# Kernel optimization log

Hardware: AMD Instinct MI355X
Metric: run time of the kernel (lower is better)

Reference implementation:

```python
import jax, jax.numpy as jnp
import numpy as np

C = 1.0        # curvature
MARGIN = 0.2
NEG_WEIGHT = 0.5
EPS = 1e-15


def poincare_dist(x, y):
    # faithful to Poincare.poincare_dist (including the odd clamp on the ratio)
    x2 = jnp.minimum((x * x).sum(-1), (1.0 - 1e-06) / C)
    y2 = jnp.minimum((y * y).sum(-1), (1.0 - 1e-06) / C)
    diff2 = ((x - y) ** 2).sum(-1)
    num = 2 * C * diff2
    den = (1 - C * x2) * (1 - C * y2)
    z = 1 + jnp.maximum(num / jnp.maximum(den, EPS), 1 + 1e-07)
    return jnp.arccosh(z)


def setup_inputs() -> dict:
    key = jax.random.key(0)
    k1, k2, k3, k4 = jax.random.split(key, 4)
    B, N, L, dh, A = 64, 16, 1024, 64, 8
    # scale so points lie well inside the unit Poincare ball
    h_curr = jax.random.normal(k1, (B, dh), dtype=jnp.float32) * 0.05
    demo_h = jax.random.normal(k2, (B, N, L, dh), dtype=jnp.float32) * 0.05
    n_idx = jax.random.randint(k3, (B, A), 0, N)
    l_idx = jax.random.randint(k4, (B, A), 0, L)  # some lt = l+lookahead will be invalid
    align_idx = jnp.stack([n_idx, l_idx], axis=-1).astype(jnp.int64)
    return {"h_curr": h_curr, "demo_h": demo_h, "align_idx": align_idx, "lookahead": 2}


def reference(h_curr, demo_h, align_idx, lookahead):
    B, dh = h_curr.shape
    _, N, L, _ = demo_h.shape
    A = align_idx.shape[1]

    n0 = align_idx[..., 0].reshape(-1)                     # [B*A]
    l0 = align_idx[..., 1].reshape(-1)
    lt = l0 + lookahead
    valid = (lt >= 0) & (lt < L)                           # [B*A]
    bb = jnp.repeat(jnp.arange(B), A)                      # [B*A]
    lt_c = jnp.clip(lt, 0, L - 1)

    h_now = h_curr[bb]                                     # [B*A, dh]
    h_tgt = demo_h[bb, n0, lt_c]                           # [B*A, dh]
    d_pos = poincare_dist(h_now, h_tgt)                    # [B*A]

    vf = valid.astype(h_curr.dtype)
    n_valid = vf.sum()
    pos_term = (d_pos * vf).sum() / jnp.maximum(n_valid, 1.0)

    # negatives: all steps strictly after lt on the same (b, n) sequence
    seq = demo_h[bb, n0]                                   # [B*A, L, dh]
    d_negs = poincare_dist(h_now[:, None, :], seq)         # [B*A, L]
    neg_mask = (jnp.arange(L)[None, :] > lt[:, None]) & valid[:, None]
    nm = neg_mask.astype(h_curr.dtype)
    hinge = jax.nn.relu(MARGIN - d_negs + d_pos[:, None]) * nm
    cnt = nm.sum(-1)                                       # [B*A]
    per_sample = hinge.sum(-1) / jnp.maximum(cnt, 1.0)
    has_neg = (cnt > 0).astype(h_curr.dtype)
    n_neg_samples = has_neg.sum()
    neg_term = (per_sample * has_neg).sum() / jnp.maximum(n_neg_samples, 1.0)

    return pos_term + NEG_WEIGHT * neg_term
```

## Files before the change

kernel.cpp:

```cpp
#include <hip/hip_runtime.h>
#include <math.h>

#define MARGIN 0.2f
#define NEG_WEIGHT 0.5f

constexpr int Bc = 64, Nc = 16, Lc = 1024, DH = 64, Ac = 8;
constexpr int NSAMP = Bc * Ac;
constexpr int CHUNKS = 16;
constexpr int ROWS_PER_CHUNK = Lc / CHUNKS;
constexpr int WPB = 4;
constexpr int GRID = NSAMP * CHUNKS / WPB;

__device__ __forceinline__ float fast_acosh(float z) {
    return __logf(z + __builtin_sqrtf(z * z - 1.0f));
}

__device__ __forceinline__ float pdist(float x2, float y2, float d2) {
    x2 = fminf(x2, 0.999999f);
    y2 = fminf(y2, 0.999999f);
    float num = 2.0f * d2;
    float den = (1.0f - x2) * (1.0f - y2);
    float ratio = num * __builtin_amdgcn_rcpf(fmaxf(den, 1e-15f));
    float z = 1.0f + fmaxf(ratio, 1.0f + 1e-7f);
    return fast_acosh(z);
}

__global__ __launch_bounds__(256) void sample_kernel(
    const float* __restrict__ h_curr,
    const float* __restrict__ demo_h,
    const int*   __restrict__ align_idx,
    const int*   __restrict__ lookahead_p,
    float* __restrict__ ws)
{
    const int tid  = threadIdx.x;
    const int task = blockIdx.x * WPB + (tid >> 6);
    const int s    = task >> 4;
    const int c    = task & 15;
    const int b    = s >> 3;
    const int lane = tid & 63;
    const int quad = lane & 3;
    const int rg   = lane >> 2;

    const int n0 = align_idx[s * 2 + 0];
    const int l0 = align_idx[s * 2 + 1];
    const int lk = lookahead_p[0];
    const int lt = l0 + lk;
    const bool valid = (lt >= 0) && (lt < Lc);

    if (!valid) {
        if (lane == 0) {
            float* wneg = ws + (size_t)(s * CHUNKS + c) * 2;
            wneg[0] = 0.0f; wneg[1] = 0.0f;
            if (c == 0) {
                float* wpos = ws + (size_t)NSAMP * CHUNKS * 2 + (size_t)s * 2;
                wpos[0] = 0.0f; wpos[1] = 0.0f;
            }
        }
        return;
    }

    const bool dead = (c * ROWS_PER_CHUNK + (ROWS_PER_CHUNK - 1)) <= lt;
    if (dead && c != 0) {
        if (lane == 0) {
            float* wneg = ws + (size_t)(s * CHUNKS + c) * 2;
            wneg[0] = 0.0f; wneg[1] = 0.0f;
        }
        return;
    }

    const int lt_c = min(max(lt, 0), Lc - 1);

    const float* __restrict__ xrow = h_curr + (size_t)b * DH + quad * 16;
    const float* __restrict__ seq  = demo_h + (((size_t)b * Nc + (size_t)n0) * Lc) * DH;

    float4 xv[4];
    #pragma unroll
    for (int j = 0; j < 4; ++j)
        xv[j] = *reinterpret_cast<const float4*>(xrow + j * 4);

    float x2 = 0.0f;
    #pragma unroll
    for (int j = 0; j < 4; ++j) {
        x2 = fmaf(xv[j].x, xv[j].x, x2);
        x2 = fmaf(xv[j].y, xv[j].y, x2);
        x2 = fmaf(xv[j].z, xv[j].z, x2);
        x2 = fmaf(xv[j].w, xv[j].w, x2);
    }
    x2 += __shfl_xor(x2, 1, 64);
    x2 += __shfl_xor(x2, 2, 64);

    float d_pos;
    {
        const float* rowp = seq + (size_t)lt_c * DH + quad * 16;
        float d2 = 0.0f, y2 = 0.0f;
        #pragma unroll
        for (int j = 0; j < 4; ++j) {
            float4 yv = *reinterpret_cast<const float4*>(rowp + j * 4);
            float dx = xv[j].x - yv.x, dy = xv[j].y - yv.y;
            float dz = xv[j].z - yv.z, dw = xv[j].w - yv.w;
            d2 = fmaf(dx, dx, d2); d2 = fmaf(dy, dy, d2);
            d2 = fmaf(dz, dz, d2); d2 = fmaf(dw, dw, d2);
            y2 = fmaf(yv.x, yv.x, y2); y2 = fmaf(yv.y, yv.y, y2);
            y2 = fmaf(yv.z, yv.z, y2); y2 = fmaf(yv.w, yv.w, y2);
        }
        d2 += __shfl_xor(d2, 1, 64); d2 += __shfl_xor(d2, 2, 64);
        y2 += __shfl_xor(y2, 1, 64); y2 += __shfl_xor(y2, 2, 64);
        d_pos = pdist(x2, y2, d2);
    }

    if (dead) {
        if (lane == 0) {
            float* wneg = ws + (size_t)(s * CHUNKS + c) * 2;
            wneg[0] = 0.0f; wneg[1] = 0.0f;
            float* wpos = ws + (size_t)NSAMP * CHUNKS * 2 + (size_t)s * 2;
            wpos[0] = d_pos; wpos[1] = 1.0f;
        }
        return;
    }

    float hinge_acc = 0.0f, cnt_acc = 0.0f;
    #pragma unroll
    for (int it = 0; it < 4; ++it) {
        const int row = c * ROWS_PER_CHUNK + it * 16 + rg;
        const float* rowp = seq + (size_t)row * DH + quad * 16;
        float d2 = 0.0f, y2 = 0.0f;
        #pragma unroll
        for (int j = 0; j < 4; ++j) {
            float4 yv = *reinterpret_cast<const float4*>(rowp + j * 4);
            float dx = xv[j].x - yv.x, dy = xv[j].y - yv.y;
            float dz = xv[j].z - yv.z, dw = xv[j].w - yv.w;
            d2 = fmaf(dx, dx, d2); d2 = fmaf(dy, dy, d2);
            d2 = fmaf(dz, dz, d2); d2 = fmaf(dw, dw, d2);
            y2 = fmaf(yv.x, yv.x, y2); y2 = fmaf(yv.y, yv.y, y2);
            y2 = fmaf(yv.z, yv.z, y2); y2 = fmaf(yv.w, yv.w, y2);
        }
        d2 += __shfl_xor(d2, 1, 64); d2 += __shfl_xor(d2, 2, 64);
        y2 += __shfl_xor(y2, 1, 64); y2 += __shfl_xor(y2, 2, 64);
        float dneg = pdist(x2, y2, d2);
        if (row > lt) {
            hinge_acc += fmaxf(MARGIN - dneg + d_pos, 0.0f);
            cnt_acc   += 1.0f;
        }
    }

    #pragma unroll
    for (int m = 4; m < 64; m <<= 1) {
        hinge_acc += __shfl_xor(hinge_acc, m, 64);
        cnt_acc   += __shfl_xor(cnt_acc,   m, 64);
    }

    if (lane == 0) {
        float* wneg = ws + (size_t)(s * CHUNKS + c) * 2;
        wneg[0] = hinge_acc;
        wneg[1] = cnt_acc;
        if (c == 0) {
            float* wpos = ws + (size_t)NSAMP * CHUNKS * 2 + (size_t)s * 2;
            wpos[0] = d_pos; wpos[1] = 1.0f;
        }
    }
}

__global__ __launch_bounds__(256) void reduce_kernel(
    const float* __restrict__ ws, float* __restrict__ out)
{
    const int tid = threadIdx.x;
    float pn = 0.0f, pv = 0.0f, nn = 0.0f, nc = 0.0f;
    for (int s = tid; s < NSAMP; s += 256) {
        float h = 0.0f, ct = 0.0f;
        #pragma unroll
        for (int c = 0; c < CHUNKS; ++c) {
            h  += ws[(size_t)(s * CHUNKS + c) * 2 + 0];
            ct += ws[(size_t)(s * CHUNKS + c) * 2 + 1];
        }
        float per_sample = h / fmaxf(ct, 1.0f);
        float has_neg = (ct > 0.0f) ? 1.0f : 0.0f;
        nn += per_sample * has_neg;
        nc += has_neg;
        pn += ws[(size_t)NSAMP * CHUNKS * 2 + (size_t)s * 2 + 0];
        pv += ws[(size_t)NSAMP * CHUNKS * 2 + (size_t)s * 2 + 1];
    }
    __shared__ float4 sh[256];
    sh[tid] = make_float4(pn, pv, nn, nc);
    __syncthreads();
    for (int off = 128; off > 0; off >>= 1) {
        if (tid < off) {
            sh[tid].x += sh[tid + off].x;
            sh[tid].y += sh[tid + off].y;
            sh[tid].z += sh[tid + off].z;
            sh[tid].w += sh[tid + off].w;
        }
        __syncthreads();
    }
    if (tid == 0) {
        float pos_term = sh[0].x / fmaxf(sh[0].y, 1.0f);
        float neg_term = sh[0].z / fmaxf(sh[0].w, 1.0f);
        out[0] = pos_term + NEG_WEIGHT * neg_term;
    }
}

extern "C" void kernel_launch(void* const* d_in, const int* in_sizes, int n_in,
                              void* d_out, int out_size, void* d_ws, size_t ws_size,
                              hipStream_t stream) {
    const float* h_curr    = (const float*)d_in[0];
    const float* demo_h    = (const float*)d_in[1];
    const int*   align_idx = (const int*)d_in[2];
    const int*   lookahead = (const int*)d_in[3];
    float* out = (float*)d_out;
    float* ws  = (float*)d_ws;

    sample_kernel<<<GRID, 256, 0, stream>>>(h_curr, demo_h, align_idx, lookahead, ws);
    reduce_kernel<<<1, 256, 0, stream>>>(ws, out);
}
```

Baseline: 24.51 us.

## Assign one full row per lane for negative distances, compute count analytically

The negative-distance loop now gives each lane one whole 64-float row instead of splitting rows across 4-lane quads over 4 iterations. This removes the per-row quad shuffles and turns the count accumulation into a closed-form computation. The cost is that each lane's loads are strided by 256 bytes, which hurts coalescing, and x is reloaded from global memory or cache in full by every lane. Accumulation is split across two chains to expose ILP.

```diff
diff --git a/kernel.cpp b/kernel.cpp
--- a/kernel.cpp
+++ b/kernel.cpp
@@ -7,7 +7,7 @@
 constexpr int Bc = 64, Nc = 16, Lc = 1024, DH = 64, Ac = 8;
 constexpr int NSAMP = Bc * Ac;
 constexpr int CHUNKS = 16;
-constexpr int ROWS_PER_CHUNK = Lc / CHUNKS;
+constexpr int RPC = Lc / CHUNKS;
 constexpr int WPB = 4;
 constexpr int GRID = NSAMP * CHUNKS / WPB;
 
@@ -39,7 +39,6 @@
     const int b    = s >> 3;
     const int lane = tid & 63;
     const int quad = lane & 3;
-    const int rg   = lane >> 2;
 
     const int n0 = align_idx[s * 2 + 0];
     const int l0 = align_idx[s * 2 + 1];
@@ -59,7 +58,7 @@
         return;
     }
 
-    const bool dead = (c * ROWS_PER_CHUNK + (ROWS_PER_CHUNK - 1)) <= lt;
+    const bool dead = (c * RPC + (RPC - 1)) <= lt;
     if (dead && c != 0) {
         if (lane == 0) {
             float* wneg = ws + (size_t)(s * CHUNKS + c) * 2;
@@ -70,13 +69,14 @@
 
     const int lt_c = min(max(lt, 0), Lc - 1);
 
-    const float* __restrict__ xrow = h_curr + (size_t)b * DH + quad * 16;
-    const float* __restrict__ seq  = demo_h + (((size_t)b * Nc + (size_t)n0) * Lc) * DH;
+    const float* __restrict__ xrow_q = h_curr + (size_t)b * DH + quad * 16;
+    const float* __restrict__ xrow   = h_curr + (size_t)b * DH;
+    const float* __restrict__ seq    = demo_h + (((size_t)b * Nc + (size_t)n0) * Lc) * DH;
 
     float4 xv[4];
     #pragma unroll
     for (int j = 0; j < 4; ++j)
-        xv[j] = *reinterpret_cast<const float4*>(xrow + j * 4);
+        xv[j] = *reinterpret_cast<const float4*>(xrow_q + j * 4);
 
     float x2 = 0.0f;
     #pragma unroll
@@ -118,41 +118,55 @@
         return;
     }
 
-    float hinge_acc = 0.0f, cnt_acc = 0.0f;
+    const int row = c * RPC + lane;
+    const float* __restrict__ rowp = seq + (size_t)row * DH;
+    const float ma = MARGIN + d_pos;
+
+    float d2a = 0.0f, d2b = 0.0f, y2a = 0.0f, y2b = 0.0f;
+    #pragma unroll 2
+    for (int dd = 0; dd < 4; ++dd) {
+        float4 xb0 = *reinterpret_cast<const float4*>(xrow + dd * 16 + 0);
+        float4 xb1 = *reinterpret_cast<const float4*>(xrow + dd * 16 + 4);
+        float4 xb2 = *reinterpret_cast<const float4*>(xrow + dd * 16 + 8);
+        float4 xb3 = *reinterpret_cast<const float4*>(xrow + dd * 16 + 12);
+        float4 yb0 = *reinterpret_cast<const float4*>(rowp + dd * 16 + 0);
+        float4 yb1 = *reinterpret_cast<const float4*>(rowp + dd * 16 + 4);
+        float4 yb2 = *reinterpret_cast<const float4*>(rowp + dd * 16 + 8);
+        float4 yb3 = *reinterpret_cast<const float4*>(rowp + dd * 16 + 12);
+
+        float dx;
+        dx = xb0.x - yb0.x; d2a = fmaf(dx, dx, d2a); y2a = fmaf(yb0.x, yb0.x, y2a);
+        dx = xb0.y - yb0.y; d2b = fmaf(dx, dx, d2b); y2b = fmaf(yb0.y, yb0.y, y2b);
+        dx = xb0.z - yb0.z; d2a = fmaf(dx, dx, d2a); y2a = fmaf(yb0.z, yb0.z, y2a);
+        dx = xb0.w - yb0.w; d2b = fmaf(dx, dx, d2b); y2b = fmaf(yb0.w, yb0.w, y2b);
+        dx = xb1.x - yb1.x; d2a = fmaf(dx, dx, d2a); y2a = fmaf(yb1.x, yb1.x, y2a);
+        dx = xb1.y - yb1.y; d2b = fmaf(dx, dx, d2b); y2b = fmaf(yb1.y, yb1.y, y2b);
+        dx = xb1.z - yb1.z; d2a = fmaf(dx, dx, d2a); y2a = fmaf(yb1.z, yb1.z, y2a);
+        dx = xb1.w - yb1.w; d2b = fmaf(dx, dx, d2b); y2b = fmaf(yb1.w, yb1.w, y2b);
+        dx = xb2.x - yb2.x; d2a = fmaf(dx, dx, d2a); y2a = fmaf(yb2.x, yb2.x, y2a);
+        dx = xb2.y - yb2.y; d2b = fmaf(dx, dx, d2b); y2b = fmaf(yb2.y, yb2.y, y2b);
+        dx = xb2.z - yb2.z; d2a = fmaf(dx, dx, d2a); y2a = fmaf(yb2.z, yb2.z, y2a);
+        dx = xb2.w - yb2.w; d2b = fmaf(dx, dx, d2b); y2b = fmaf(yb2.w, yb2.w, y2b);
+        dx = xb3.x - yb3.x; d2a = fmaf(dx, dx, d2a); y2a = fmaf(yb3.x, yb3.x, y2a);
+        dx = xb3.y - yb3.y; d2b = fmaf(dx, dx, d2b); y2b = fmaf(yb3.y, yb3.y, y2b);
+        dx = xb3.z - yb3.z; d2a = fmaf(dx, dx, d2a); y2a = fmaf(yb3.z, yb3.z, y2a);
+        dx = xb3.w - yb3.w; d2b = fmaf(dx, dx, d2b); y2b = fmaf(yb3.w, yb3.w, y2b);
+    }
+    const float d2 = d2a + d2b;
+    const float y2 = y2a + y2b;
+
+    const float dneg = pdist(x2, y2, d2);
+    float h = ((row > lt) ? fmaxf(ma - dneg, 0.0f) : 0.0f);
+
     #pragma unroll
-    for (int it = 0; it < 4; ++it) {
-        const int row = c * ROWS_PER_CHUNK + it * 16 + rg;
-        const float* rowp = seq + (size_t)row * DH + quad * 16;
-        float d2 = 0.0f, y2 = 0.0f;
-        #pragma unroll
-        for (int j = 0; j < 4; ++j) {
-            float4 yv = *reinterpret_cast<const float4*>(rowp + j * 4);
-            float dx = xv[j].x - yv.x, dy = xv[j].y - yv.y;
-            float dz = xv[j].z - yv.z, dw = xv[j].w - yv.w;
-            d2 = fmaf(dx, dx, d2); d2 = fmaf(dy, dy, d2);
-            d2 = fmaf(dz, dz, d2); d2 = fmaf(dw, dw, d2);
-            y2 = fmaf(yv.x, yv.x, y2); y2 = fmaf(yv.y, yv.y, y2);
-            y2 = fmaf(yv.z, yv.z, y2); y2 = fmaf(yv.w, yv.w, y2);
-        }
-        d2 += __shfl_xor(d2, 1, 64); d2 += __shfl_xor(d2, 2, 64);
-        y2 += __shfl_xor(y2, 1, 64); y2 += __shfl_xor(y2, 2, 64);
-        float dneg = pdist(x2, y2, d2);
-        if (row > lt) {
-            hinge_acc += fmaxf(MARGIN - dneg + d_pos, 0.0f);
-            cnt_acc   += 1.0f;
-        }
-    }
-
-    #pragma unroll
-    for (int m = 4; m < 64; m <<= 1) {
-        hinge_acc += __shfl_xor(hinge_acc, m, 64);
-        cnt_acc   += __shfl_xor(cnt_acc,   m, 64);
-    }
+    for (int m = 1; m < 64; m <<= 1)
+        h += __shfl_xor(h, m, 64);
 
     if (lane == 0) {
+        const int cnt = (c + 1) * RPC - max(c * RPC, lt + 1);
         float* wneg = ws + (size_t)(s * CHUNKS + c) * 2;
-        wneg[0] = hinge_acc;
-        wneg[1] = cnt_acc;
+        wneg[0] = h;
+        wneg[1] = (float)cnt;
         if (c == 0) {
             float* wpos = ws + (size_t)NSAMP * CHUNKS * 2 + (size_t)s * 2;
             wpos[0] = d_pos; wpos[1] = 1.0f;
```

New measurement: 33.65 us. +37.3%, slower.

## Remap lanes to 16 per row and skip dead row groups in chunk

Applied to the files above, without the earlier changes.

Each row of 64 floats is now handled by 16 lanes with one float4 each instead of 4 lanes with 16 floats, so a wavefront covers 4 rows per iteration over 16 iterations. Row groups lying entirely at or before the target step are skipped. The negative count is computed in closed form instead of being reduced across lanes. This cuts registers per thread and wasted distance evaluations in partially dead chunks, at the cost of two extra shuffle stages per reduction and a longer, branchy loop.

```diff
diff --git a/kernel.cpp b/kernel.cpp
--- a/kernel.cpp
+++ b/kernel.cpp
@@ -7,7 +7,7 @@
 constexpr int Bc = 64, Nc = 16, Lc = 1024, DH = 64, Ac = 8;
 constexpr int NSAMP = Bc * Ac;
 constexpr int CHUNKS = 16;
-constexpr int ROWS_PER_CHUNK = Lc / CHUNKS;
+constexpr int RPC = Lc / CHUNKS;
 constexpr int WPB = 4;
 constexpr int GRID = NSAMP * CHUNKS / WPB;
 
@@ -38,8 +38,8 @@
     const int c    = task & 15;
     const int b    = s >> 3;
     const int lane = tid & 63;
-    const int quad = lane & 3;
-    const int rg   = lane >> 2;
+    const int gl   = lane & 15;
+    const int rg   = lane >> 4;
 
     const int n0 = align_idx[s * 2 + 0];
     const int l0 = align_idx[s * 2 + 1];
@@ -59,7 +59,7 @@
         return;
     }
 
-    const bool dead = (c * ROWS_PER_CHUNK + (ROWS_PER_CHUNK - 1)) <= lt;
+    const bool dead = (c * RPC + (RPC - 1)) <= lt;
     if (dead && c != 0) {
         if (lane == 0) {
             float* wneg = ws + (size_t)(s * CHUNKS + c) * 2;
@@ -70,41 +70,26 @@
 
     const int lt_c = min(max(lt, 0), Lc - 1);
 
-    const float* __restrict__ xrow = h_curr + (size_t)b * DH + quad * 16;
+    const float* __restrict__ xrow = h_curr + (size_t)b * DH;
     const float* __restrict__ seq  = demo_h + (((size_t)b * Nc + (size_t)n0) * Lc) * DH;
 
-    float4 xv[4];
-    #pragma unroll
-    for (int j = 0; j < 4; ++j)
-        xv[j] = *reinterpret_cast<const float4*>(xrow + j * 4);
-
-    float x2 = 0.0f;
-    #pragma unroll
-    for (int j = 0; j < 4; ++j) {
-        x2 = fmaf(xv[j].x, xv[j].x, x2);
-        x2 = fmaf(xv[j].y, xv[j].y, x2);
-        x2 = fmaf(xv[j].z, xv[j].z, x2);
-        x2 = fmaf(xv[j].w, xv[j].w, x2);
-    }
+    const float4 xq = *reinterpret_cast<const float4*>(xrow + gl * 4);
+    float x2 = fmaf(xq.x, xq.x, fmaf(xq.y, xq.y, fmaf(xq.z, xq.z, xq.w * xq.w)));
     x2 += __shfl_xor(x2, 1, 64);
     x2 += __shfl_xor(x2, 2, 64);
+    x2 += __shfl_xor(x2, 4, 64);
+    x2 += __shfl_xor(x2, 8, 64);
 
     float d_pos;
     {
-        const float* rowp = seq + (size_t)lt_c * DH + quad * 16;
-        float d2 = 0.0f, y2 = 0.0f;
-        #pragma unroll
-        for (int j = 0; j < 4; ++j) {
-            float4 yv = *reinterpret_cast<const float4*>(rowp + j * 4);
-            float dx = xv[j].x - yv.x, dy = xv[j].y - yv.y;
-            float dz = xv[j].z - yv.z, dw = xv[j].w - yv.w;
-            d2 = fmaf(dx, dx, d2); d2 = fmaf(dy, dy, d2);
-            d2 = fmaf(dz, dz, d2); d2 = fmaf(dw, dw, d2);
-            y2 = fmaf(yv.x, yv.x, y2); y2 = fmaf(yv.y, yv.y, y2);
-            y2 = fmaf(yv.z, yv.z, y2); y2 = fmaf(yv.w, yv.w, y2);
-        }
+        const float4 tv = *reinterpret_cast<const float4*>(seq + (size_t)lt_c * DH + gl * 4);
+        float dx = xq.x - tv.x, dy = xq.y - tv.y, dz = xq.z - tv.z, dw = xq.w - tv.w;
+        float d2 = fmaf(dx, dx, fmaf(dy, dy, fmaf(dz, dz, dw * dw)));
+        float y2 = fmaf(tv.x, tv.x, fmaf(tv.y, tv.y, fmaf(tv.z, tv.z, tv.w * tv.w)));
         d2 += __shfl_xor(d2, 1, 64); d2 += __shfl_xor(d2, 2, 64);
+        d2 += __shfl_xor(d2, 4, 64); d2 += __shfl_xor(d2, 8, 64);
         y2 += __shfl_xor(y2, 1, 64); y2 += __shfl_xor(y2, 2, 64);
+        y2 += __shfl_xor(y2, 4, 64); y2 += __shfl_xor(y2, 8, 64);
         d_pos = pdist(x2, y2, d2);
     }
 
@@ -118,41 +103,33 @@
         return;
     }
 
-    float hinge_acc = 0.0f, cnt_acc = 0.0f;
+    const float ma = MARGIN + d_pos;
+    float h = 0.0f;
     #pragma unroll
-    for (int it = 0; it < 4; ++it) {
-        const int row = c * ROWS_PER_CHUNK + it * 16 + rg;
-        const float* rowp = seq + (size_t)row * DH + quad * 16;
-        float d2 = 0.0f, y2 = 0.0f;
-        #pragma unroll
-        for (int j = 0; j < 4; ++j) {
-            float4 yv = *reinterpret_cast<const float4*>(rowp + j * 4);
-            float dx = xv[j].x - yv.x, dy = xv[j].y - yv.y;
-            float dz = xv[j].z - yv.z, dw = xv[j].w - yv.w;
-            d2 = fmaf(dx, dx, d2); d2 = fmaf(dy, dy, d2);
-            d2 = fmaf(dz, dz, d2); d2 = fmaf(dw, dw, d2);
-            y2 = fmaf(yv.x, yv.x, y2); y2 = fmaf(yv.y, yv.y, y2);
-            y2 = fmaf(yv.z, yv.z, y2); y2 = fmaf(yv.w, yv.w, y2);
-        }
+    for (int it = 0; it < 16; ++it) {
+        const int rowbase = c * RPC + it * 4;
+        if (rowbase + 3 <= lt) continue;
+        const int row = rowbase + rg;
+        const float4 yv = *reinterpret_cast<const float4*>(seq + (size_t)row * DH + gl * 4);
+        float dx = xq.x - yv.x, dy = xq.y - yv.y, dz = xq.z - yv.z, dw = xq.w - yv.w;
+        float d2 = fmaf(dx, dx, fmaf(dy, dy, fmaf(dz, dz, dw * dw)));
+        float y2 = fmaf(yv.x, yv.x, fmaf(yv.y, yv.y, fmaf(yv.z, yv.z, yv.w * yv.w)));
         d2 += __shfl_xor(d2, 1, 64); d2 += __shfl_xor(d2, 2, 64);
+        d2 += __shfl_xor(d2, 4, 64); d2 += __shfl_xor(d2, 8, 64);
         y2 += __shfl_xor(y2, 1, 64); y2 += __shfl_xor(y2, 2, 64);
-        float dneg = pdist(x2, y2, d2);
-        if (row > lt) {
-            hinge_acc += fmaxf(MARGIN - dneg + d_pos, 0.0f);
-            cnt_acc   += 1.0f;
-        }
+        y2 += __shfl_xor(y2, 4, 64); y2 += __shfl_xor(y2, 8, 64);
+        const float dneg = pdist(x2, y2, d2);
+        h += (row > lt) ? fmaxf(ma - dneg, 0.0f) : 0.0f;
     }
 
-    #pragma unroll
-    for (int m = 4; m < 64; m <<= 1) {
-        hinge_acc += __shfl_xor(hinge_acc, m, 64);
-        cnt_acc   += __shfl_xor(cnt_acc,   m, 64);
-    }
+    h += __shfl_xor(h, 16, 64);
+    h += __shfl_xor(h, 32, 64);
 
     if (lane == 0) {
+        const int cnt = (c + 1) * RPC - max(c * RPC, lt + 1);
         float* wneg = ws + (size_t)(s * CHUNKS + c) * 2;
-        wneg[0] = hinge_acc;
-        wneg[1] = cnt_acc;
+        wneg[0] = h;
+        wneg[1] = (float)cnt;
         if (c == 0) {
             float* wpos = ws + (size_t)NSAMP * CHUNKS * 2 + (size_t)s * 2;
             wpos[0] = d_pos; wpos[1] = 1.0f;
```

Result: slower. 26.88 us (+9.7%).

## Transpose workspace layout, compute neg counts analytically, and use single-pass wave reduce

Applied to the files above, without the earlier changes.

Stores per-chunk hinge sums in a chunk-major layout so the reduce kernel reads them coalesced. Negative counts are no longer accumulated and stored; the reduce kernel derives them from lt. The reduce kernel now uses 512 threads with one sample per thread and wave shuffles instead of a shared-memory tree. The task-to-block mapping is also interleaved so the four waves of a block come from different samples, which may balance dead chunks across CUs but loses locality within a block.

```diff
diff --git a/kernel.cpp b/kernel.cpp
--- a/kernel.cpp
+++ b/kernel.cpp
@@ -7,7 +7,7 @@
 constexpr int Bc = 64, Nc = 16, Lc = 1024, DH = 64, Ac = 8;
 constexpr int NSAMP = Bc * Ac;
 constexpr int CHUNKS = 16;
-constexpr int ROWS_PER_CHUNK = Lc / CHUNKS;
+constexpr int RPC = Lc / CHUNKS;
 constexpr int WPB = 4;
 constexpr int GRID = NSAMP * CHUNKS / WPB;
 
@@ -30,10 +30,11 @@
     const float* __restrict__ demo_h,
     const int*   __restrict__ align_idx,
     const int*   __restrict__ lookahead_p,
-    float* __restrict__ ws)
+    float* __restrict__ wneg,
+    float* __restrict__ wpos)
 {
     const int tid  = threadIdx.x;
-    const int task = blockIdx.x * WPB + (tid >> 6);
+    const int task = (tid >> 6) * GRID + blockIdx.x;
     const int s    = task >> 4;
     const int c    = task & 15;
     const int b    = s >> 3;
@@ -49,22 +50,15 @@
 
     if (!valid) {
         if (lane == 0) {
-            float* wneg = ws + (size_t)(s * CHUNKS + c) * 2;
-            wneg[0] = 0.0f; wneg[1] = 0.0f;
-            if (c == 0) {
-                float* wpos = ws + (size_t)NSAMP * CHUNKS * 2 + (size_t)s * 2;
-                wpos[0] = 0.0f; wpos[1] = 0.0f;
-            }
+            wneg[c * NSAMP + s] = 0.0f;
+            if (c == 0) wpos[s] = 0.0f;
         }
         return;
     }
 
-    const bool dead = (c * ROWS_PER_CHUNK + (ROWS_PER_CHUNK - 1)) <= lt;
+    const bool dead = (c * RPC + (RPC - 1)) <= lt;
     if (dead && c != 0) {
-        if (lane == 0) {
-            float* wneg = ws + (size_t)(s * CHUNKS + c) * 2;
-            wneg[0] = 0.0f; wneg[1] = 0.0f;
-        }
+        if (lane == 0) wneg[c * NSAMP + s] = 0.0f;
         return;
     }
 
@@ -110,18 +104,16 @@
 
     if (dead) {
         if (lane == 0) {
-            float* wneg = ws + (size_t)(s * CHUNKS + c) * 2;
-            wneg[0] = 0.0f; wneg[1] = 0.0f;
-            float* wpos = ws + (size_t)NSAMP * CHUNKS * 2 + (size_t)s * 2;
-            wpos[0] = d_pos; wpos[1] = 1.0f;
+            wneg[c * NSAMP + s] = 0.0f;
+            wpos[s] = d_pos;
         }
         return;
     }
 
-    float hinge_acc = 0.0f, cnt_acc = 0.0f;
+    float hinge_acc = 0.0f;
     #pragma unroll
     for (int it = 0; it < 4; ++it) {
-        const int row = c * ROWS_PER_CHUNK + it * 16 + rg;
+        const int row = c * RPC + it * 16 + rg;
         const float* rowp = seq + (size_t)row * DH + quad * 16;
         float d2 = 0.0f, y2 = 0.0f;
         #pragma unroll
@@ -137,63 +129,66 @@
         d2 += __shfl_xor(d2, 1, 64); d2 += __shfl_xor(d2, 2, 64);
         y2 += __shfl_xor(y2, 1, 64); y2 += __shfl_xor(y2, 2, 64);
         float dneg = pdist(x2, y2, d2);
-        if (row > lt) {
+        if (row > lt)
             hinge_acc += fmaxf(MARGIN - dneg + d_pos, 0.0f);
-            cnt_acc   += 1.0f;
-        }
-    }
-
-    #pragma unroll
-    for (int m = 4; m < 64; m <<= 1) {
-        hinge_acc += __shfl_xor(hinge_acc, m, 64);
-        cnt_acc   += __shfl_xor(cnt_acc,   m, 64);
-    }
+    }
+
+    hinge_acc += __shfl_xor(hinge_acc, 4, 64);
+    hinge_acc += __shfl_xor(hinge_acc, 8, 64);
+    hinge_acc += __shfl_xor(hinge_acc, 16, 64);
+    hinge_acc += __shfl_xor(hinge_acc, 32, 64);
 
     if (lane == 0) {
-        float* wneg = ws + (size_t)(s * CHUNKS + c) * 2;
-        wneg[0] = hinge_acc;
-        wneg[1] = cnt_acc;
-        if (c == 0) {
-            float* wpos = ws + (size_t)NSAMP * CHUNKS * 2 + (size_t)s * 2;
-            wpos[0] = d_pos; wpos[1] = 1.0f;
-        }
-    }
-}
-
-__global__ __launch_bounds__(256) void reduce_kernel(
-    const float* __restrict__ ws, float* __restrict__ out)
+        wneg[c * NSAMP + s] = hinge_acc;
+        if (c == 0) wpos[s] = d_pos;
+    }
+}
+
+__global__ __launch_bounds__(512) void reduce_kernel(
+    const float* __restrict__ wneg,
+    const float* __restrict__ wpos,
+    const int*   __restrict__ align_idx,
+    const int*   __restrict__ lookahead_p,
+    float* __restrict__ out)
 {
     const int tid = threadIdx.x;
-    float pn = 0.0f, pv = 0.0f, nn = 0.0f, nc = 0.0f;
-    for (int s = tid; s < NSAMP; s += 256) {
-        float h = 0.0f, ct = 0.0f;
+    const int lk = lookahead_p[0];
+
+    const int lt = align_idx[tid * 2 + 1] + lk;
+    const bool v = (lt >= 0) && (lt < Lc);
+
+    float h = 0.0f;
+    #pragma unroll
+    for (int c = 0; c < CHUNKS; ++c)
+        h += wneg[c * NSAMP + tid];
+
+    const float cnt = v ? (float)(Lc - 1 - lt) : 0.0f;
+    const float has_neg = (cnt > 0.0f) ? 1.0f : 0.0f;
+
+    float pn = wpos[tid];
+    float pv = v ? 1.0f : 0.0f;
+    float nn = (h / fmaxf(cnt, 1.0f)) * has_neg;
+    float nc = has_neg;
+
+    #pragma unroll
+    for (int m = 1; m < 64; m <<= 1) {
+        pn += __shfl_xor(pn, m, 64);
+        pv += __shfl_xor(pv, m, 64);
+        nn += __shfl_xor(nn, m, 64);
+        nc += __shfl_xor(nc, m, 64);
+    }
+
+    __shared__ float4 sh[8];
+    if ((tid & 63) == 0) sh[tid >> 6] = make_float4(pn, pv, nn, nc);
+    __syncthreads();
+    if (tid == 0) {
+        float4 a = sh[0];
         #pragma unroll
-        for (int c = 0; c < CHUNKS; ++c) {
-            h  += ws[(size_t)(s * CHUNKS + c) * 2 + 0];
-            ct += ws[(size_t)(s * CHUNKS + c) * 2 + 1];
-        }
-        float per_sample = h / fmaxf(ct, 1.0f);
-        float has_neg = (ct > 0.0f) ? 1.0f : 0.0f;
-        nn += per_sample * has_neg;
-        nc += has_neg;
-        pn += ws[(size_t)NSAMP * CHUNKS * 2 + (size_t)s * 2 + 0];
-        pv += ws[(size_t)NSAMP * CHUNKS * 2 + (size_t)s * 2 + 1];
-    }
-    __shared__ float4 sh[256];
-    sh[tid] = make_float4(pn, pv, nn, nc);
-    __syncthreads();
-    for (int off = 128; off > 0; off >>= 1) {
-        if (tid < off) {
-            sh[tid].x += sh[tid + off].x;
-            sh[tid].y += sh[tid + off].y;
-            sh[tid].z += sh[tid + off].z;
-            sh[tid].w += sh[tid + off].w;
-        }
-        __syncthreads();
-    }
-    if (tid == 0) {
-        float pos_term = sh[0].x / fmaxf(sh[0].y, 1.0f);
-        float neg_term = sh[0].z / fmaxf(sh[0].w, 1.0f);
+        for (int w = 1; w < 8; ++w) {
+            a.x += sh[w].x; a.y += sh[w].y; a.z += sh[w].z; a.w += sh[w].w;
+        }
+        const float pos_term = a.x / fmaxf(a.y, 1.0f);
+        const float neg_term = a.z / fmaxf(a.w, 1.0f);
         out[0] = pos_term + NEG_WEIGHT * neg_term;
     }
 }
@@ -205,9 +200,11 @@
     const float* demo_h    = (const float*)d_in[1];
     const int*   align_idx = (const int*)d_in[2];
     const int*   lookahead = (const int*)d_in[3];
-    float* out = (float*)d_out;
-    float* ws  = (float*)d_ws;
-
-    sample_kernel<<<GRID, 256, 0, stream>>>(h_curr, demo_h, align_idx, lookahead, ws);
-    reduce_kernel<<<1, 256, 0, stream>>>(ws, out);
-}
+    float* out  = (float*)d_out;
+    float* wneg = (float*)d_ws;
+    float* wpos = (float*)d_ws + CHUNKS * NSAMP;
+
+    sample_kernel<<<GRID, 256, 0, stream>>>(
+        h_curr, demo_h, align_idx, lookahead, wneg, wpos);
+    reduce_kernel<<<1, 512, 0, stream>>>(wneg, wpos, align_idx, lookahead, out);
+}
```

New measurement: 24.08 us (median of 2 runs). About the same (-1.7%).
